# Kernel optimization log

Hardware: AMD Instinct MI355X
Metric: run time of the kernel (lower is better)

The kernel has to match this reference:

```python
import jax, jax.numpy as jnp
import numpy as np

GRID_SPACING = 1.0


def setup_inputs() -> dict:
    key = jax.random.key(0)
    k1, k2 = jax.random.split(key)
    B, H, W, D = 4, 128, 128, 128
    phi_positive = jax.random.normal(k1, (B, H, W, D), dtype=jnp.float32)
    phi_negative = jax.random.uniform(k2, (B, H, W, D), dtype=jnp.float32)
    lambda_repulsion = jnp.ones((1,), dtype=jnp.float32) * 2.0
    return {
        "phi_positive": phi_positive,
        "phi_negative": phi_negative,
        "lambda_repulsion": lambda_repulsion,
    }


def reference(phi_positive, phi_negative, lambda_repulsion):
    h = GRID_SPACING
    # Conformal factor Phi = phi+ - lambda * phi-
    Phi = phi_positive - lambda_repulsion[0] * phi_negative  # (B,H,W,D)
    # Single replicate-pad of Phi, reused for gradient and Laplacian stencils
    p = jnp.pad(Phi, ((0, 0), (1, 1), (1, 1), (1, 1)), mode="edge")
    xp = p[:, 2:, 1:-1, 1:-1]
    xm = p[:, :-2, 1:-1, 1:-1]
    yp = p[:, 1:-1, 2:, 1:-1]
    ym = p[:, 1:-1, :-2, 1:-1]
    zp = p[:, 1:-1, 1:-1, 2:]
    zm = p[:, 1:-1, 1:-1, :-2]
    inv2h = 1.0 / (2.0 * h)
    gx = (xp - xm) * inv2h
    gy = (yp - ym) * inv2h
    gz = (zp - zm) * inv2h
    grad_sq = gx * gx + gy * gy + gz * gz  # |grad Phi|^2
    lap = (xp + xm + yp + ym + zp + zm - 6.0 * Phi) / (h * h)
    # R = -2 e^{-2Phi} (lap Phi + 2 |grad Phi|^2)
    R = -2.0 * jnp.exp(-2.0 * Phi) * (lap + 2.0 * grad_sq)
    return R
```

## Files before the change

kernel.cpp:

```cpp
#include <hip/hip_runtime.h>


#define NVEC (4 * 128 * 128 * 32)

__global__ __launch_bounds__(256) void conformal_kernel(
    const float* __restrict__ pos, const float* __restrict__ neg,
    const float* __restrict__ lamp, float* __restrict__ out)
{
    const float lam = lamp[0];
    const int vid = blockIdx.x * blockDim.x + threadIdx.x;
    if (vid >= NVEC) return;

    const int dvec = vid & 31;
    const int w    = (vid >> 5)  & 127;
    const int h    = (vid >> 12) & 127;

    const float4* posv = (const float4*)pos;
    const float4* negv = (const float4*)neg;

    const int i_yp = (w < 127) ? vid + 32   : vid;
    const int i_ym = (w > 0)   ? vid - 32   : vid;
    const int i_xp = (h < 127) ? vid + 4096 : vid;
    const int i_xm = (h > 0)   ? vid - 4096 : vid;

    float4 p_c  = posv[vid],  n_c  = negv[vid];
    float4 p_yp = posv[i_yp], n_yp = negv[i_yp];
    float4 p_ym = posv[i_ym], n_ym = negv[i_ym];
    float4 p_xp = posv[i_xp], n_xp = negv[i_xp];
    float4 p_xm = posv[i_xm], n_xm = negv[i_xm];

    const int fbase = vid << 2;
    float pl = 0.f, nl = 0.f, pr = 0.f, nr = 0.f;
    if (dvec > 0)  { pl = pos[fbase - 1]; nl = neg[fbase - 1]; }
    if (dvec < 31) { pr = pos[fbase + 4]; nr = neg[fbase + 4]; }

    float c[4];
    c[0] = p_c.x - lam * n_c.x;
    c[1] = p_c.y - lam * n_c.y;
    c[2] = p_c.z - lam * n_c.z;
    c[3] = p_c.w - lam * n_c.w;

    const float left  = (dvec > 0)  ? (pl - lam * nl) : c[0];
    const float right = (dvec < 31) ? (pr - lam * nr) : c[3];

    float xpv[4], xmv[4], ypv[4], ymv[4];
    xpv[0] = p_xp.x - lam * n_xp.x;  xpv[1] = p_xp.y - lam * n_xp.y;
    xpv[2] = p_xp.z - lam * n_xp.z;  xpv[3] = p_xp.w - lam * n_xp.w;
    xmv[0] = p_xm.x - lam * n_xm.x;  xmv[1] = p_xm.y - lam * n_xm.y;
    xmv[2] = p_xm.z - lam * n_xm.z;  xmv[3] = p_xm.w - lam * n_xm.w;
    ypv[0] = p_yp.x - lam * n_yp.x;  ypv[1] = p_yp.y - lam * n_yp.y;
    ypv[2] = p_yp.z - lam * n_yp.z;  ypv[3] = p_yp.w - lam * n_yp.w;
    ymv[0] = p_ym.x - lam * n_ym.x;  ymv[1] = p_ym.y - lam * n_ym.y;
    ymv[2] = p_ym.z - lam * n_ym.z;  ymv[3] = p_ym.w - lam * n_ym.w;

    const float zl[4] = { left, c[0], c[1], c[2] };
    const float zr[4] = { c[1], c[2], c[3], right };

    float r[4];
#pragma unroll
    for (int j = 0; j < 4; ++j) {
        const float gx = (xpv[j] - xmv[j]) * 0.5f;
        const float gy = (ypv[j] - ymv[j]) * 0.5f;
        const float gz = (zr[j]  - zl[j])  * 0.5f;
        const float grad_sq = gx * gx + gy * gy + gz * gz;
        const float lap = xpv[j] + xmv[j] + ypv[j] + ymv[j] + zl[j] + zr[j]
                          - 6.0f * c[j];
        r[j] = -2.0f * __expf(-2.0f * c[j]) * (lap + 2.0f * grad_sq);
    }

    float4 o;
    o.x = r[0]; o.y = r[1]; o.z = r[2]; o.w = r[3];
    ((float4*)out)[vid] = o;
}

extern "C" void kernel_launch(void* const* d_in, const int* in_sizes, int n_in,
                              void* d_out, int out_size, void* d_ws, size_t ws_size,
                              hipStream_t stream) {
    const float* pos = (const float*)d_in[0];
    const float* neg = (const float*)d_in[1];
    const float* lam = (const float*)d_in[2];
    float* out = (float*)d_out;

    const int threads = 256;
    const int blocks  = NVEC / threads;
    conformal_kernel<<<blocks, threads, 0, stream>>>(pos, neg, lam, out);
}
```

Before: 107.8 us.

## Get z-neighbours via warp shuffles, use nontemporal stores, drop bounds check

After: 115.1 us. 1.07x slower.

```diff
diff --git a/kernel.cpp b/kernel.cpp
--- a/kernel.cpp
+++ b/kernel.cpp
@@ -2,6 +2,8 @@
 
 
 #define NVEC (4 * 128 * 128 * 32)
+
+typedef float vfloat4 __attribute__((ext_vector_type(4)));
 
 __global__ __launch_bounds__(256) void conformal_kernel(
     const float* __restrict__ pos, const float* __restrict__ neg,
@@ -9,54 +11,47 @@
 {
     const float lam = lamp[0];
     const int vid = blockIdx.x * blockDim.x + threadIdx.x;
-    if (vid >= NVEC) return;
 
     const int dvec = vid & 31;
     const int w    = (vid >> 5)  & 127;
     const int h    = (vid >> 12) & 127;
 
-    const float4* posv = (const float4*)pos;
-    const float4* negv = (const float4*)neg;
+    const vfloat4* posv = (const vfloat4*)pos;
+    const vfloat4* negv = (const vfloat4*)neg;
 
     const int i_yp = (w < 127) ? vid + 32   : vid;
     const int i_ym = (w > 0)   ? vid - 32   : vid;
     const int i_xp = (h < 127) ? vid + 4096 : vid;
     const int i_xm = (h > 0)   ? vid - 4096 : vid;
 
-    float4 p_c  = posv[vid],  n_c  = negv[vid];
-    float4 p_yp = posv[i_yp], n_yp = negv[i_yp];
-    float4 p_ym = posv[i_ym], n_ym = negv[i_ym];
-    float4 p_xp = posv[i_xp], n_xp = negv[i_xp];
-    float4 p_xm = posv[i_xm], n_xm = negv[i_xm];
+    vfloat4 p_c  = posv[vid],  n_c  = negv[vid];
+    vfloat4 p_yp = posv[i_yp], n_yp = negv[i_yp];
+    vfloat4 p_ym = posv[i_ym], n_ym = negv[i_ym];
+    vfloat4 p_xp = posv[i_xp], n_xp = negv[i_xp];
+    vfloat4 p_xm = posv[i_xm], n_xm = negv[i_xm];
 
-    const int fbase = vid << 2;
-    float pl = 0.f, nl = 0.f, pr = 0.f, nr = 0.f;
-    if (dvec > 0)  { pl = pos[fbase - 1]; nl = neg[fbase - 1]; }
-    if (dvec < 31) { pr = pos[fbase + 4]; nr = neg[fbase + 4]; }
+    const vfloat4 cphi = p_c - lam * n_c;
+    const float c0 = cphi.x, c1 = cphi.y, c2 = cphi.z, c3 = cphi.w;
 
-    float c[4];
-    c[0] = p_c.x - lam * n_c.x;
-    c[1] = p_c.y - lam * n_c.y;
-    c[2] = p_c.z - lam * n_c.z;
-    c[3] = p_c.w - lam * n_c.w;
+    const float from_up   = __shfl_up(c3, 1);
+    const float from_down = __shfl_down(c0, 1);
+    const float left  = (dvec > 0)  ? from_up   : c0;
+    const float right = (dvec < 31) ? from_down : c3;
 
-    const float left  = (dvec > 0)  ? (pl - lam * nl) : c[0];
-    const float right = (dvec < 31) ? (pr - lam * nr) : c[3];
+    const vfloat4 xp = p_xp - lam * n_xp;
+    const vfloat4 xm = p_xm - lam * n_xm;
+    const vfloat4 yp = p_yp - lam * n_yp;
+    const vfloat4 ym = p_ym - lam * n_ym;
 
-    float xpv[4], xmv[4], ypv[4], ymv[4];
-    xpv[0] = p_xp.x - lam * n_xp.x;  xpv[1] = p_xp.y - lam * n_xp.y;
-    xpv[2] = p_xp.z - lam * n_xp.z;  xpv[3] = p_xp.w - lam * n_xp.w;
-    xmv[0] = p_xm.x - lam * n_xm.x;  xmv[1] = p_xm.y - lam * n_xm.y;
-    xmv[2] = p_xm.z - lam * n_xm.z;  xmv[3] = p_xm.w - lam * n_xm.w;
-    ypv[0] = p_yp.x - lam * n_yp.x;  ypv[1] = p_yp.y - lam * n_yp.y;
-    ypv[2] = p_yp.z - lam * n_yp.z;  ypv[3] = p_yp.w - lam * n_yp.w;
-    ymv[0] = p_ym.x - lam * n_ym.x;  ymv[1] = p_ym.y - lam * n_ym.y;
-    ymv[2] = p_ym.z - lam * n_ym.z;  ymv[3] = p_ym.w - lam * n_ym.w;
+    const float cc[4]  = { c0, c1, c2, c3 };
+    const float zl[4]  = { left, c0, c1, c2 };
+    const float zr[4]  = { c1, c2, c3, right };
+    const float xpv[4] = { xp.x, xp.y, xp.z, xp.w };
+    const float xmv[4] = { xm.x, xm.y, xm.z, xm.w };
+    const float ypv[4] = { yp.x, yp.y, yp.z, yp.w };
+    const float ymv[4] = { ym.x, ym.y, ym.z, ym.w };
 
-    const float zl[4] = { left, c[0], c[1], c[2] };
-    const float zr[4] = { c[1], c[2], c[3], right };
-
-    float r[4];
+    vfloat4 o;
 #pragma unroll
     for (int j = 0; j < 4; ++j) {
         const float gx = (xpv[j] - xmv[j]) * 0.5f;
@@ -64,13 +59,11 @@
         const float gz = (zr[j]  - zl[j])  * 0.5f;
         const float grad_sq = gx * gx + gy * gy + gz * gz;
         const float lap = xpv[j] + xmv[j] + ypv[j] + ymv[j] + zl[j] + zr[j]
-                          - 6.0f * c[j];
-        r[j] = -2.0f * __expf(-2.0f * c[j]) * (lap + 2.0f * grad_sq);
+                          - 6.0f * cc[j];
+        o[j] = -2.0f * __expf(-2.0f * cc[j]) * (lap + 2.0f * grad_sq);
     }
 
-    float4 o;
-    o.x = r[0]; o.y = r[1]; o.z = r[2]; o.w = r[3];
-    ((float4*)out)[vid] = o;
+    __builtin_nontemporal_store(o, ((vfloat4*)out) + vid);
 }
 
 extern "C" void kernel_launch(void* const* d_in, const int* in_sizes, int n_in,
```
